# Kernel tuning notes

Measured on AMD Instinct MI355X. Metric: run time of the kernel, lower is better.

The kernel has to match this reference:

```python
import jax, jax.numpy as jnp
import numpy as np

N_CELLS = 10   # nr_cells
CELL = 20      # cell_size (w)
R = 1          # read heads
HID = 128      # controller hidden
IN = 10        # dnc input_size
OUT = 10       # output_dim
CLIP = 20.0
IFACE = R * CELL + 3 * CELL + 5 * R + 3  # 88


def _lstm_step(x, h, c, Wih, Whh, b):
    gates = x @ Wih.T + h @ Whh.T + b
    i, f, g, o = jnp.split(gates, 4, axis=-1)
    c = jax.nn.sigmoid(f) * c + jax.nn.sigmoid(i) * jnp.tanh(g)
    h = jax.nn.sigmoid(o) * jnp.tanh(c)
    return h, c


def _content(mem, keys, strengths):
    # mem (b,n,w), keys (b,k,w), strengths (b,k) -> (b,k,n)
    dot = jnp.einsum('bkw,bnw->bkn', keys, mem)
    kn = jnp.linalg.norm(keys, axis=-1, keepdims=True)
    mn = jnp.linalg.norm(mem, axis=-1)[:, None, :]
    return jax.nn.softmax(dot / (kn * mn + 1e-6) * strengths[..., None], axis=-1)


def _allocate(usage):
    u = 1e-6 + (1.0 - 1e-6) * usage
    idx = jnp.argsort(u, axis=-1)                      # ascending usage
    su = jnp.take_along_axis(u, idx, axis=-1)
    excl = jnp.concatenate([jnp.ones_like(su[:, :1]), jnp.cumprod(su, axis=-1)[:, :-1]], axis=-1)
    sa = (1.0 - su) * excl                             # sorted allocation weights
    inv = jnp.argsort(idx, axis=-1)
    return jnp.take_along_axis(sa, inv, axis=-1)


def _dnc_forward(x, W_ih0, W_hh0, b0, W_ih1, W_hh1, b1, W_if, b_if, W_out, b_out):
    B, T, _ = x.shape
    dt = x.dtype
    z = lambda *s: jnp.zeros(s, dt)
    carry0 = (z(B, HID), z(B, HID), z(B, HID), z(B, HID),   # h0,c0,h1,c1
              z(B, N_CELLS, CELL),                          # memory
              z(B, N_CELLS),                                # usage
              z(B, N_CELLS),                                # precedence
              z(B, N_CELLS, N_CELLS),                       # link matrix
              z(B, R, N_CELLS),                             # read weights
              z(B, N_CELLS),                                # write weights
              z(B, R, CELL))                                # read vectors
    eye = jnp.eye(N_CELLS, dtype=dt)

    def step(carry, xt):
        h0, c0, h1, c1, mem, usage, prec, link, rw, ww, rv = carry
        inp = jnp.concatenate([xt, rv.reshape(B, R * CELL)], axis=-1)
        h0, c0 = _lstm_step(inp, h0, c0, W_ih0, W_hh0, b0)
        h1, c1 = _lstm_step(h0, h1, c1, W_ih1, W_hh1, b1)
        ctrl = jnp.clip(h1, -CLIP, CLIP)
        xi = ctrl @ W_if.T + b_if                            # (B, 88)
        rk = jnp.tanh(xi[:, 0:20]).reshape(B, R, CELL)       # read keys
        rs = jax.nn.softplus(xi[:, 20:21])                   # read strengths
        wk = jnp.tanh(xi[:, 21:41]).reshape(B, 1, CELL)      # write key
        ws = jax.nn.softplus(xi[:, 41:42])                   # write strength
        er = jax.nn.sigmoid(xi[:, 42:62])                    # erase vector
        wv = jnp.tanh(xi[:, 62:82])                          # write vector
        fg = jax.nn.sigmoid(xi[:, 82:83])                    # free gates
        ga = jax.nn.sigmoid(xi[:, 83:84])                    # allocation gate
        gw = jax.nn.sigmoid(xi[:, 84:85])                    # write gate
        modes = jax.nn.softmax(xi[:, 85:88].reshape(B, R, 3), axis=-1)
        # --- write ---
        psi = jnp.prod(1.0 - fg[:, :, None] * rw, axis=1)    # retention (b,n)
        usage = (usage + ww - usage * ww) * psi
        alloc = _allocate(usage)
        cw = _content(mem, wk, ws)[:, 0]                     # (b,n)
        ww = gw * (ga * alloc + (1.0 - ga) * cw)
        mem = mem * (1.0 - ww[:, :, None] * er[:, None, :]) + ww[:, :, None] * wv[:, None, :]
        link = (1.0 - ww[:, :, None] - ww[:, None, :]) * link + ww[:, :, None] * prec[:, None, :]
        link = link * (1.0 - eye)
        prec = (1.0 - ww.sum(-1, keepdims=True)) * prec + ww
        # --- read ---
        fwd_w = jnp.einsum('brn,bmn->brm', rw, link)         # L @ w  (forward)
        bwd_w = jnp.einsum('brn,bnm->brm', rw, link)         # L^T @ w (backward)
        cr = _content(mem, rk, rs)
        rw = modes[..., 0:1] * bwd_w + modes[..., 1:2] * cr + modes[..., 2:3] * fwd_w
        rv = jnp.einsum('brn,bnw->brw', rw, mem)
        o = jnp.concatenate([ctrl, rv.reshape(B, R * CELL)], axis=-1)
        y = o @ W_out.T + b_out
        return (h0, c0, h1, c1, mem, usage, prec, link, rw, ww, rv), y

    _, ys = jax.lax.scan(step, carry0, jnp.swapaxes(x, 0, 1))
    return ys[-1]  # output[:, -1, :]


def setup_inputs() -> dict:
    key = jax.random.key(0)
    ks = jax.random.split(key, 8)
    s = 0.08
    B, T = 512, 512
    return {
        'x': jax.random.normal(ks[0], (B, T, IN), jnp.float32),
        'W_ih0': s * jax.random.normal(ks[1], (4 * HID, IN + R * CELL), jnp.float32),
        'W_hh0': s * jax.random.normal(ks[2], (4 * HID, HID), jnp.float32),
        'b0': jnp.zeros((4 * HID,), jnp.float32),
        'W_ih1': s * jax.random.normal(ks[3], (4 * HID, HID), jnp.float32),
        'W_hh1': s * jax.random.normal(ks[4], (4 * HID, HID), jnp.float32),
        'b1': jnp.zeros((4 * HID,), jnp.float32),
        'W_if': s * jax.random.normal(ks[5], (IFACE, HID), jnp.float32),
        'b_if': jnp.zeros((IFACE,), jnp.float32),
        'W_out': s * jax.random.normal(ks[6], (OUT, HID + R * CELL), jnp.float32),
        'b_out': jnp.zeros((OUT,), jnp.float32),
    }


def reference(x, W_ih0, W_hh0, b0, W_ih1, W_hh1, b1, W_if, b_if, W_out, b_out):
    return _dnc_forward(x, W_ih0, W_hh0, b0, W_ih1, W_hh1, b1, W_if, b_if, W_out, b_out)
```

## Files before the change

kernel.cpp:

```cpp
#include <hip/hip_runtime.h>
#include <math.h>

#define NT 512
#define NB 512
#define HID 128
#define NIN 10
#define NC 10
#define CW 20
#define NIF 88
#define NOUT 10
#define GB 16
#define BLK 512
#define NWG (NB/GB)

typedef _Float16 h1;
typedef _Float16 h8 __attribute__((ext_vector_type(8)));
typedef float f32x4 __attribute__((ext_vector_type(4)));

__device__ __forceinline__ float rcpf(float x) { return __builtin_amdgcn_rcpf(x); }
__device__ __forceinline__ float sigf(float x) { return rcpf(1.0f + __expf(-x)); }
__device__ __forceinline__ float tanhf_(float x) {
  float xc = fminf(fmaxf(x, -15.f), 15.f);
  float e = __expf(2.f * xc);
  return (e - 1.f) * rcpf(e + 1.f);
}
__device__ __forceinline__ float splus(float x) { return fmaxf(x, 0.0f) + __logf(1.f + __expf(-fabsf(x))); }

__device__ __forceinline__ float bq0(float v) { return __builtin_bit_cast(float, __builtin_amdgcn_ds_swizzle(__builtin_bit_cast(int, v), 0x001C)); }
__device__ __forceinline__ float bq1(float v) { return __builtin_bit_cast(float, __builtin_amdgcn_ds_swizzle(__builtin_bit_cast(int, v), 0x003C)); }
__device__ __forceinline__ float bq2(float v) { return __builtin_bit_cast(float, __builtin_amdgcn_ds_swizzle(__builtin_bit_cast(int, v), 0x005C)); }
__device__ __forceinline__ float bq3(float v) { return __builtin_bit_cast(float, __builtin_amdgcn_ds_swizzle(__builtin_bit_cast(int, v), 0x007C)); }

__device__ __forceinline__ f32x4 mfma16(float4 a, float4 b, f32x4 c) {
  return __builtin_amdgcn_mfma_f32_16x16x32_f16(
      __builtin_bit_cast(h8, a), __builtin_bit_cast(h8, b), c, 0, 0, 0);
}

__device__ __forceinline__ float4 pack8(const float* p) {
  h1 v[8];
  #pragma unroll
  for (int j = 0; j < 8; ++j) v[j] = (h1)p[j];
  return *reinterpret_cast<float4*>(v);
}

__device__ __host__ __forceinline__ int origrow(int prow) { return (prow & 3) * 128 + (prow >> 2); }

__global__ __launch_bounds__(256) void dnc_packf_kernel(
    const float* __restrict__ Whh0, const float* __restrict__ Wih1,
    const float* __restrict__ Whh1, float4* __restrict__ ws)
{
  int i = blockIdx.x * 256 + threadIdx.x;
  if (i >= 384 * 64) return;
  int l = i & 63, frag = i >> 6;
  int m = frag >> 7, f = frag & 127;
  int nt = f >> 2, kt = f & 3;
  int r = origrow(nt * 16 + (l & 15));
  int k0 = kt * 32 + (l >> 4) * 8;
  const float* W = (m == 0) ? Whh0 : (m == 1) ? Wih1 : Whh1;
  ws[i] = pack8(W + (size_t)r * HID + k0);
}

__global__ __launch_bounds__(BLK)
void dnc_mfma_kernel(
    const float* __restrict__ x,
    const float* __restrict__ Wih0, const float* __restrict__ Whh0, const float* __restrict__ b0,
    const float* __restrict__ Wih1, const float* __restrict__ Whh1, const float* __restrict__ b1,
    const float* __restrict__ Wif,  const float* __restrict__ bif,
    const float* __restrict__ Wout, const float* __restrict__ bout,
    const float4* __restrict__ wsT,
    float* __restrict__ out)
{
  __shared__ __align__(16) float4 s_w0f[32*64];
  __shared__ __align__(16) float4 s_wiff[24*64];
  __shared__ __align__(16) h1 s_h0f[16*16*8];
  __shared__ __align__(16) h1 s_h1f[16*16*8];
  __shared__ __align__(16) h1 s_ctf[16*16*8];
  __shared__ __align__(16) h1 s_inpf[4*16*8];
  __shared__ float s_c0[GB][HID], s_c1[GB][HID];
  __shared__ float s_ctrl32[GB][HID];
  __shared__ float s_mem[GB][NC][CW];
  __shared__ float s_link[GB][NC][NC];
  __shared__ float s_rk[GB][CW], s_wk[GB][CW], s_er[GB][CW], s_wv[GB][CW];
  __shared__ float s_sc[GB][8], s_mraw[GB][4];
  __shared__ float s_usage[GB][NC], s_u[GB][NC], s_prec[GB][NC], s_prec2[GB][NC];
  __shared__ float s_rw[GB][NC], s_ww[GB][NC], s_cw[GB][NC], s_cr[GB][NC];
  __shared__ float s_fwd[GB][NC], s_bwd[GB][NC];
  __shared__ float s_rv[GB][CW];

  const int tid = threadIdx.x;
  const int l = tid & 63, w = tid >> 6;
  const int col = l & 15, g4 = l >> 4, q4 = l & 3;
  const int bbase = blockIdx.x * GB;

  for (int idx = tid; idx < 32*64; idx += BLK) {
    int nt = idx >> 6, ll = idx & 63;
    int r = origrow(nt*16 + (ll & 15));
    int kg = ll >> 4;
    float tmp[8];
    #pragma unroll
    for (int j = 0; j < 8; ++j) {
      int k = kg*8 + j;
      int cc = (k < 10) ? k : ((k < 12) ? -1 : (k - 2));
      tmp[j] = (cc < 0) ? 0.f : Wih0[r*(NIN+CW) + cc];
    }
    s_w0f[idx] = pack8(tmp);
  }
  for (int idx = tid; idx < 24*64; idx += BLK) {
    int f = idx >> 6, ll = idx & 63;
    int nt = f >> 2, kt = f & 3;
    int q = nt*16 + (ll & 15);
    int k0 = kt*32 + (ll >> 4)*8;
    float tmp[8];
    #pragma unroll
    for (int j = 0; j < 8; ++j) tmp[j] = (q < NIF) ? Wif[q*HID + k0 + j] : 0.f;
    s_wiff[idx] = pack8(tmp);
  }
  for (int idx = tid; idx < 16*16*8; idx += BLK) {
    s_h0f[idx] = (h1)0.f; s_h1f[idx] = (h1)0.f; s_ctf[idx] = (h1)0.f;
  }
  if (tid < 4*16*8) s_inpf[tid] = (h1)0.f;
  for (int idx = tid; idx < GB*HID; idx += BLK) { int b = idx >> 7, u = idx & 127;
    s_c0[b][u] = 0.f; s_c1[b][u] = 0.f; s_ctrl32[b][u] = 0.f; }
  for (int idx = tid; idx < GB*NC*CW; idx += BLK) { int b = idx/(NC*CW), e = idx%(NC*CW);
    s_mem[b][e/CW][e%CW] = 0.f; }
  for (int idx = tid; idx < GB*NC*NC; idx += BLK) { int b = idx/(NC*NC), e = idx%(NC*NC);
    s_link[b][e/NC][e%NC] = 0.f; }
  if (tid < GB*NC) { int b = tid & 15, n = tid >> 4;
    s_usage[b][n] = 0.f; s_prec[b][n] = 0.f; s_rw[b][n] = 0.f; s_ww[b][n] = 0.f; }
  for (int idx = tid; idx < GB*CW; idx += BLK) { int b = idx/CW, c = idx%CW; s_rv[b][c] = 0.f; }
  if (tid < GB*NIN) { int b = tid/NIN, i = tid - b*NIN;
    float v = x[((size_t)(bbase+b)*NT + 0)*NIN + i];
    s_inpf[((i>>3)*16 + b)*8 + (i&7)] = (h1)v;
  }
  const float b0v0 = b0[origrow((w*4+0)*16+col)], b0v1 = b0[origrow((w*4+1)*16+col)];
  const float b0v2 = b0[origrow((w*4+2)*16+col)], b0v3 = b0[origrow((w*4+3)*16+col)];
  const float b1v0 = b1[origrow((w*4+0)*16+col)], b1v1 = b1[origrow((w*4+1)*16+col)];
  const float b1v2 = b1[origrow((w*4+2)*16+col)], b1v3 = b1[origrow((w*4+3)*16+col)];
  float bifv = 0.f;
  if (w < 6) { int q = w*16 + col; bifv = (q < NIF) ? bif[q] : 0.f; }
  __syncthreads();

  const float4* h0fp = (const float4*)s_h0f;
  const float4* h1fp = (const float4*)s_h1f;
  const float4* ctfp = (const float4*)s_ctf;
  const float4* inpfp = (const float4*)s_inpf;

  auto dnc_phases = [&](bool run) {
    if (run) {
      if (tid < GB*NC) {
        int b = tid & 15, n = tid >> 4;
        float fg = s_sc[b][2];
        float psi = 1.f - fg * s_rw[b][n];
        float u = s_usage[b][n], wq = s_ww[b][n];
        u = (u + wq - u*wq) * psi;
        s_usage[b][n] = u;
        s_u[b][n] = 1e-6f + (1.0f - 1e-6f) * u;
        float dot = 0.f, mn = 0.f, kn = 0.f;
        #pragma unroll
        for (int c = 0; c < CW; ++c) {
          float m = s_mem[b][n][c], k = s_wk[b][c];
          dot += k*m; mn += m*m; kn += k*k;
        }
        s_cw[b][n] = dot * rcpf(sqrtf(kn)*sqrtf(mn) + 1e-6f) * s_sc[b][1];
      } else if (tid < GB*NC + GB) {
        int b = tid - GB*NC;
        float m0 = s_mraw[b][0], m1 = s_mraw[b][1], m2 = s_mraw[b][2];
        float mm = fmaxf(m0, fmaxf(m1, m2));
        float e0 = __expf(m0-mm), e1 = __expf(m1-mm), e2 = __expf(m2-mm);
        float es = rcpf(e0+e1+e2);
        s_sc[b][5] = e0*es; s_sc[b][6] = e1*es; s_sc[b][7] = e2*es;
      }
    }
    __syncthreads();
    if (run && tid < GB*NC) {
      int b = tid & 15, n = tid >> 4;
      float mx = -1e30f;
      #pragma unroll
      for (int m = 0; m < NC; ++m) mx = fmaxf(mx, s_cw[b][m]);
      float sm = 0.f;
      #pragma unroll
      for (int m = 0; m < NC; ++m) sm += __expf(s_cw[b][m]-mx);
      float cwv = __expf(s_cw[b][n]-mx) * rcpf(sm);
      float un = s_u[b][n];
      float excl = 1.f;
      #pragma unroll
      for (int m = 0; m < NC; ++m) {
        float um = s_u[b][m];
        bool before = (um < un) || (um == un && m < n);
        excl *= before ? um : 1.f;
      }
      float alloc = (1.f - un) * excl;
      float ga = s_sc[b][3], gw = s_sc[b][4];
      s_ww[b][n] = gw * (ga*alloc + (1.f-ga)*cwv);
    }
    __syncthreads();
    if (run) {
      for (int e = tid; e < GB*NC*CW; e += BLK) {
        int b = e/(NC*CW), rr = (e/CW) % NC, c = e % CW;
        float wq = s_ww[b][rr];
        s_mem[b][rr][c] = s_mem[b][rr][c]*(1.f - wq*s_er[b][c]) + wq*s_wv[b][c];
      }
      for (int e = tid; e < GB*NC*NC; e += BLK) {
        int b = e/(NC*NC), i2 = (e/NC) % NC, j2 = e % NC;
        float wi = s_ww[b][i2], wj = s_ww[b][j2];
        float ln = (1.f - wi - wj)*s_link[b][i2][j2] + wi*s_prec[b][j2];
        s_link[b][i2][j2] = (i2==j2) ? 0.f : ln;
      }
      if (tid < GB*NC) {
        int b = tid & 15, n = tid >> 4;
        float sw2 = 0.f;
        #pragma unroll
        for (int m = 0; m < NC; ++m) sw2 += s_ww[b][m];
        s_prec2[b][n] = (1.f - sw2)*s_prec[b][n] + s_ww[b][n];
      }
    }
    __syncthreads();
    if (run) {
      if (tid < GB*NC) {
        int b = tid & 15, m = tid >> 4;
        s_prec[b][m] = s_prec2[b][m];
        float a = 0.f;
        #pragma unroll
        for (int n = 0; n < NC; ++n) a += s_rw[b][n]*s_link[b][m][n];
        s_fwd[b][m] = a;
      } else if (tid < 2*GB*NC) {
        int tt = tid - GB*NC, b = tt & 15, m = tt >> 4;
        float a = 0.f;
        #pragma unroll
        for (int n = 0; n < NC; ++n) a += s_rw[b][n]*s_link[b][n][m];
        s_bwd[b][m] = a;
      } else if (tid < 3*GB*NC) {
        int tt = tid - 2*GB*NC, b = tt & 15, n = tt >> 4;
        float dot = 0.f, mn = 0.f, kn = 0.f;
        #pragma unroll
        for (int c = 0; c < CW; ++c) {
          float m = s_mem[b][n][c], k = s_rk[b][c];
          dot += k*m; mn += m*m; kn += k*k;
        }
        s_cr[b][n] = dot * rcpf(sqrtf(kn)*sqrtf(mn) + 1e-6f) * s_sc[b][0];
      }
    }
    __syncthreads();
    if (run && tid < GB*NC) {
      int b = tid & 15, n = tid >> 4;
      float mx = -1e30f;
      #pragma unroll
      for (int m = 0; m < NC; ++m) mx = fmaxf(mx, s_cr[b][m]);
      float sm = 0.f;
      #pragma unroll
      for (int m = 0; m < NC; ++m) sm += __expf(s_cr[b][m]-mx);
      float cr = __expf(s_cr[b][n]-mx)*rcpf(sm);
      s_rw[b][n] = s_sc[b][5]*s_bwd[b][n] + s_sc[b][6]*cr + s_sc[b][7]*s_fwd[b][n];
    }
    __syncthreads();
    if (run && tid < GB*CW) {
      int b = tid & 15, c = tid >> 4;
      float a = 0.f;
      #pragma unroll
      for (int n = 0; n < NC; ++n) a += s_rw[b][n]*s_mem[b][n][c];
      s_rv[b][c] = a;
      int k = 12 + c;
      s_inpf[((k>>3)*16 + b)*8 + (k&7)] = (h1)a;
    }
    __syncthreads();
  };

  auto lstm_layer = [&](f32x4 ac0, f32x4 ac1, f32x4 ac2, f32x4 ac3,
                        float (*cst)[HID], h1* hf, bool isL1) {
    float GI[4] = {0,0,0,0}, GF[4] = {0,0,0,0}, GG[4] = {0,0,0,0}, GO[4] = {0,0,0,0};
    #pragma unroll
    for (int r = 0; r < 4; ++r) {
      f32x4 A = (r==0) ? ac0 : (r==1) ? ac1 : (r==2) ? ac2 : ac3;
      #pragma unroll
      for (int i = 0; i < 4; ++i) {
        float t0 = bq0(A[i]), t1 = bq1(A[i]), t2 = bq2(A[i]), t3 = bq3(A[i]);
        GI[i] = (q4 == r) ? t0 : GI[i];
        GF[i] = (q4 == r) ? t1 : GF[i];
        GG[i] = (q4 == r) ? t2 : GG[i];
        GO[i] = (q4 == r) ? t3 : GO[i];
      }
    }
    const int u = (w*4 + q4)*4 + (col >> 2);
    #pragma unroll
    for (int i = 0; i < 4; ++i) {
      int b = g4*4 + i;
      float c = sigf(GF[i])*cst[b][u] + sigf(GI[i])*tanhf_(GG[i]);
      cst[b][u] = c;
      float h = sigf(GO[i])*tanhf_(c);
      hf[((u>>3)*16 + b)*8 + (u&7)] = (h1)h;
      if (isL1) {
        float cl = fminf(fmaxf(h, -20.f), 20.f);
        s_ctf[((u>>3)*16 + b)*8 + (u&7)] = (h1)cl;
        s_ctrl32[b][u] = cl;
      }
    }
  };

  for (int t = 0; t < NT; ++t) {
    dnc_phases(t > 0);

    unsigned lnd = 0;
    asm volatile("" : "+v"(lnd));
    const float4* WS = (const float4*)((const char*)wsT + lnd);

    float4 ai  = inpfp[g4*16 + col];
    float4 a00 = h0fp[(0*4+g4)*16 + col], a01 = h0fp[(1*4+g4)*16 + col];
    float4 a02 = h0fp[(2*4+g4)*16 + col], a03 = h0fp[(3*4+g4)*16 + col];
    float4 a10 = h1fp[(0*4+g4)*16 + col], a11 = h1fp[(1*4+g4)*16 + col];
    float4 a12 = h1fp[(2*4+g4)*16 + col], a13 = h1fp[(3*4+g4)*16 + col];

    f32x4 acc0 = {b0v0,b0v0,b0v0,b0v0}, acc1 = {b0v1,b0v1,b0v1,b0v1};
    f32x4 acc2 = {b0v2,b0v2,b0v2,b0v2}, acc3 = {b0v3,b0v3,b0v3,b0v3};
    f32x4 gcc0 = {b1v0,b1v0,b1v0,b1v0}, gcc1 = {b1v1,b1v1,b1v1,b1v1};
    f32x4 gcc2 = {b1v2,b1v2,b1v2,b1v2}, gcc3 = {b1v3,b1v3,b1v3,b1v3};

#define G0IT(ACC, IT)                                                   \
    ACC = mfma16(ai,  s_w0f[(w*4+IT)*64 + l], ACC);                     \
    ACC = mfma16(a00, WS[((w*4+IT)*4+0)*64 + l], ACC);                  \
    ACC = mfma16(a01, WS[((w*4+IT)*4+1)*64 + l], ACC);                  \
    ACC = mfma16(a02, WS[((w*4+IT)*4+2)*64 + l], ACC);                  \
    ACC = mfma16(a03, WS[((w*4+IT)*4+3)*64 + l], ACC);
    G0IT(acc0, 0) G0IT(acc1, 1) G0IT(acc2, 2) G0IT(acc3, 3)
#undef G0IT
#define G1H1(ACC, IT)                                                   \
    ACC = mfma16(a10, WS[(256+(w*4+IT)*4+0)*64 + l], ACC);              \
    ACC = mfma16(a11, WS[(256+(w*4+IT)*4+1)*64 + l], ACC);              \
    ACC = mfma16(a12, WS[(256+(w*4+IT)*4+2)*64 + l], ACC);              \
    ACC = mfma16(a13, WS[(256+(w*4+IT)*4+3)*64 + l], ACC);
    G1H1(gcc0, 0) G1H1(gcc1, 1) G1H1(gcc2, 2) G1H1(gcc3, 3)
#undef G1H1
    __syncthreads();

    lstm_layer(acc0, acc1, acc2, acc3, s_c0, s_h0f, false);
    __syncthreads();

    {
      float4 ah0 = h0fp[(0*4+g4)*16 + col], ah1 = h0fp[(1*4+g4)*16 + col];
      float4 ah2 = h0fp[(2*4+g4)*16 + col], ah3 = h0fp[(3*4+g4)*16 + col];
#define G1H0(ACC, IT)                                                   \
      ACC = mfma16(ah0, WS[(128+(w*4+IT)*4+0)*64 + l], ACC);            \
      ACC = mfma16(ah1, WS[(128+(w*4+IT)*4+1)*64 + l], ACC);            \
      ACC = mfma16(ah2, WS[(128+(w*4+IT)*4+2)*64 + l], ACC);            \
      ACC = mfma16(ah3, WS[(128+(w*4+IT)*4+3)*64 + l], ACC);
      G1H0(gcc0, 0) G1H0(gcc1, 1) G1H0(gcc2, 2) G1H0(gcc3, 3)
#undef G1H0
      lstm_layer(gcc0, gcc1, gcc2, gcc3, s_c1, s_h1f, true);
    }
    __syncthreads();

    if (w < 6) {
      float4 ac0 = ctfp[(0*4+g4)*16 + col], ac1 = ctfp[(1*4+g4)*16 + col];
      float4 ac2 = ctfp[(2*4+g4)*16 + col], ac3 = ctfp[(3*4+g4)*16 + col];
      f32x4 acc = {bifv, bifv, bifv, bifv};
      acc = mfma16(ac0, s_wiff[(w*4+0)*64 + l], acc);
      acc = mfma16(ac1, s_wiff[(w*4+1)*64 + l], acc);
      acc = mfma16(ac2, s_wiff[(w*4+2)*64 + l], acc);
      acc = mfma16(ac3, s_wiff[(w*4+3)*64 + l], acc);
      int q = w*16 + col;
      if (q < NIF) {
        #pragma unroll
        for (int i = 0; i < 4; ++i) {
          float a = acc[i];
          int b = g4*4 + i;
          if      (q < 20)  s_rk[b][q]    = tanhf_(a);
          else if (q == 20) s_sc[b][0]    = splus(a);
          else if (q < 41)  s_wk[b][q-21] = tanhf_(a);
          else if (q == 41) s_sc[b][1]    = splus(a);
          else if (q < 62)  s_er[b][q-42] = sigf(a);
          else if (q < 82)  s_wv[b][q-62] = tanhf_(a);
          else if (q == 82) s_sc[b][2]    = sigf(a);
          else if (q == 83) s_sc[b][3]    = sigf(a);
          else if (q == 84) s_sc[b][4]    = sigf(a);
          else              s_mraw[b][q-85] = a;
        }
      }
    } else {
      for (int e = (w-6)*64 + l; e < GB*NIN; e += 128) {
        int b = e/NIN, i = e - b*NIN;
        if (t+1 < NT) {
          float v = x[((size_t)(bbase+b)*NT + (t+1))*NIN + i];
          s_inpf[((i>>3)*16 + b)*8 + (i&7)] = (h1)v;
        }
      }
    }
    __syncthreads();
  }

  dnc_phases(true);

  if (tid < GB*NOUT) {
    int b = tid & 15, o = tid >> 4;
    float a = bout[o];
    const float* Wr = Wout + o*(HID+CW);
    #pragma unroll 4
    for (int k = 0; k < HID; ++k) a += Wr[k]*s_ctrl32[b][k];
    #pragma unroll
    for (int c = 0; c < CW; ++c) a += Wr[HID+c]*s_rv[b][c];
    out[(size_t)(bbase+b)*NOUT + o] = a;
  }
}

extern "C" void kernel_launch(void* const* d_in, const int* in_sizes, int n_in,
                              void* d_out, int out_size, void* d_ws, size_t ws_size,
                              hipStream_t stream) {
  (void)in_sizes; (void)n_in; (void)out_size; (void)ws_size;
  const float* x    = (const float*)d_in[0];
  const float* Wih0 = (const float*)d_in[1];
  const float* Whh0 = (const float*)d_in[2];
  const float* b0   = (const float*)d_in[3];
  const float* Wih1 = (const float*)d_in[4];
  const float* Whh1 = (const float*)d_in[5];
  const float* b1   = (const float*)d_in[6];
  const float* Wif  = (const float*)d_in[7];
  const float* bif  = (const float*)d_in[8];
  const float* Wout = (const float*)d_in[9];
  const float* bout = (const float*)d_in[10];
  float* out = (float*)d_out;
  float4* ws = (float4*)d_ws;

  dnc_packf_kernel<<<dim3(96), dim3(256), 0, stream>>>(Whh0, Wih1, Whh1, ws);
  dnc_mfma_kernel<<<dim3(NWG), dim3(BLK), 0, stream>>>(
      x, Wih0, Whh0, b0, Wih1, Whh1, b1, Wif, bif, Wout, bout, ws, out);
}
```

Measured before the change: 5.543 ms.

## Interleave per-wave DNC memory phases with LSTM MFMA recurrences, replacing block barriers

```diff
diff --git a/kernel.cpp b/kernel.cpp
--- a/kernel.cpp
+++ b/kernel.cpp
@@ -30,6 +30,9 @@
 __device__ __forceinline__ float bq1(float v) { return __builtin_bit_cast(float, __builtin_amdgcn_ds_swizzle(__builtin_bit_cast(int, v), 0x003C)); }
 __device__ __forceinline__ float bq2(float v) { return __builtin_bit_cast(float, __builtin_amdgcn_ds_swizzle(__builtin_bit_cast(int, v), 0x005C)); }
 __device__ __forceinline__ float bq3(float v) { return __builtin_bit_cast(float, __builtin_amdgcn_ds_swizzle(__builtin_bit_cast(int, v), 0x007C)); }
+
+#define LDSFENCE() do { asm volatile("s_waitcnt lgkmcnt(0)" ::: "memory"); \
+                        __builtin_amdgcn_sched_barrier(0); } while (0)
 
 __device__ __forceinline__ f32x4 mfma16(float4 a, float4 b, f32x4 c) {
   return __builtin_amdgcn_mfma_f32_16x16x32_f16(
@@ -61,7 +64,7 @@
 }
 
 __global__ __launch_bounds__(BLK)
-void dnc_mfma_kernel(
+void dnc_olap2_kernel(
     const float* __restrict__ x,
     const float* __restrict__ Wih0, const float* __restrict__ Whh0, const float* __restrict__ b0,
     const float* __restrict__ Wih1, const float* __restrict__ Whh1, const float* __restrict__ b1,
@@ -91,6 +94,7 @@
   const int l = tid & 63, w = tid >> 6;
   const int col = l & 15, g4 = l >> 4, q4 = l & 3;
   const int bbase = blockIdx.x * GB;
+  const int s = l & 31, bb = 2 * w + (l >> 5);
 
   for (int idx = tid; idx < 32*64; idx += BLK) {
     int nt = idx >> 6, ll = idx & 63;
@@ -145,124 +149,121 @@
   const float4* ctfp = (const float4*)s_ctf;
   const float4* inpfp = (const float4*)s_inpf;
 
-  auto dnc_phases = [&](bool run) {
-    if (run) {
-      if (tid < GB*NC) {
-        int b = tid & 15, n = tid >> 4;
-        float fg = s_sc[b][2];
-        float psi = 1.f - fg * s_rw[b][n];
-        float u = s_usage[b][n], wq = s_ww[b][n];
-        u = (u + wq - u*wq) * psi;
-        s_usage[b][n] = u;
-        s_u[b][n] = 1e-6f + (1.0f - 1e-6f) * u;
-        float dot = 0.f, mn = 0.f, kn = 0.f;
-        #pragma unroll
-        for (int c = 0; c < CW; ++c) {
-          float m = s_mem[b][n][c], k = s_wk[b][c];
-          dot += k*m; mn += m*m; kn += k*k;
-        }
-        s_cw[b][n] = dot * rcpf(sqrtf(kn)*sqrtf(mn) + 1e-6f) * s_sc[b][1];
-      } else if (tid < GB*NC + GB) {
-        int b = tid - GB*NC;
-        float m0 = s_mraw[b][0], m1 = s_mraw[b][1], m2 = s_mraw[b][2];
-        float mm = fmaxf(m0, fmaxf(m1, m2));
-        float e0 = __expf(m0-mm), e1 = __expf(m1-mm), e2 = __expf(m2-mm);
-        float es = rcpf(e0+e1+e2);
-        s_sc[b][5] = e0*es; s_sc[b][6] = e1*es; s_sc[b][7] = e2*es;
-      }
-    }
-    __syncthreads();
-    if (run && tid < GB*NC) {
-      int b = tid & 15, n = tid >> 4;
+  auto dncH = [&]() {
+    if (s < NC) {
+      int n = s;
+      float fg = s_sc[bb][2];
+      float psi = 1.f - fg * s_rw[bb][n];
+      float u = s_usage[bb][n], wq = s_ww[bb][n];
+      u = (u + wq - u*wq) * psi;
+      s_usage[bb][n] = u;
+      s_u[bb][n] = 1e-6f + (1.0f - 1e-6f) * u;
+      float dot = 0.f, mn = 0.f, kn = 0.f;
+      #pragma unroll
+      for (int c = 0; c < CW; ++c) {
+        float mv = s_mem[bb][n][c], kv = s_wk[bb][c];
+        dot += kv*mv; mn += mv*mv; kn += kv*kv;
+      }
+      s_cw[bb][n] = dot * rcpf(sqrtf(kn)*sqrtf(mn) + 1e-6f) * s_sc[bb][1];
+    } else if (s == NC) {
+      float m0 = s_mraw[bb][0], m1 = s_mraw[bb][1], m2 = s_mraw[bb][2];
+      float mm = fmaxf(m0, fmaxf(m1, m2));
+      float e0 = __expf(m0-mm), e1 = __expf(m1-mm), e2 = __expf(m2-mm);
+      float es = rcpf(e0+e1+e2);
+      s_sc[bb][5] = e0*es; s_sc[bb][6] = e1*es; s_sc[bb][7] = e2*es;
+    }
+  };
+  auto dncI = [&]() {
+    if (s < NC) {
+      int n = s;
       float mx = -1e30f;
       #pragma unroll
-      for (int m = 0; m < NC; ++m) mx = fmaxf(mx, s_cw[b][m]);
+      for (int m = 0; m < NC; ++m) mx = fmaxf(mx, s_cw[bb][m]);
       float sm = 0.f;
       #pragma unroll
-      for (int m = 0; m < NC; ++m) sm += __expf(s_cw[b][m]-mx);
-      float cwv = __expf(s_cw[b][n]-mx) * rcpf(sm);
-      float un = s_u[b][n];
+      for (int m = 0; m < NC; ++m) sm += __expf(s_cw[bb][m]-mx);
+      float cwv = __expf(s_cw[bb][n]-mx) * rcpf(sm);
+      float un = s_u[bb][n];
       float excl = 1.f;
       #pragma unroll
       for (int m = 0; m < NC; ++m) {
-        float um = s_u[b][m];
+        float um = s_u[bb][m];
         bool before = (um < un) || (um == un && m < n);
         excl *= before ? um : 1.f;
       }
       float alloc = (1.f - un) * excl;
-      float ga = s_sc[b][3], gw = s_sc[b][4];
-      s_ww[b][n] = gw * (ga*alloc + (1.f-ga)*cwv);
-    }
-    __syncthreads();
-    if (run) {
-      for (int e = tid; e < GB*NC*CW; e += BLK) {
-        int b = e/(NC*CW), rr = (e/CW) % NC, c = e % CW;
-        float wq = s_ww[b][rr];
-        s_mem[b][rr][c] = s_mem[b][rr][c]*(1.f - wq*s_er[b][c]) + wq*s_wv[b][c];
-      }
-      for (int e = tid; e < GB*NC*NC; e += BLK) {
-        int b = e/(NC*NC), i2 = (e/NC) % NC, j2 = e % NC;
-        float wi = s_ww[b][i2], wj = s_ww[b][j2];
-        float ln = (1.f - wi - wj)*s_link[b][i2][j2] + wi*s_prec[b][j2];
-        s_link[b][i2][j2] = (i2==j2) ? 0.f : ln;
-      }
-      if (tid < GB*NC) {
-        int b = tid & 15, n = tid >> 4;
-        float sw2 = 0.f;
-        #pragma unroll
-        for (int m = 0; m < NC; ++m) sw2 += s_ww[b][m];
-        s_prec2[b][n] = (1.f - sw2)*s_prec[b][n] + s_ww[b][n];
-      }
-    }
-    __syncthreads();
-    if (run) {
-      if (tid < GB*NC) {
-        int b = tid & 15, m = tid >> 4;
-        s_prec[b][m] = s_prec2[b][m];
-        float a = 0.f;
-        #pragma unroll
-        for (int n = 0; n < NC; ++n) a += s_rw[b][n]*s_link[b][m][n];
-        s_fwd[b][m] = a;
-      } else if (tid < 2*GB*NC) {
-        int tt = tid - GB*NC, b = tt & 15, m = tt >> 4;
-        float a = 0.f;
-        #pragma unroll
-        for (int n = 0; n < NC; ++n) a += s_rw[b][n]*s_link[b][n][m];
-        s_bwd[b][m] = a;
-      } else if (tid < 3*GB*NC) {
-        int tt = tid - 2*GB*NC, b = tt & 15, n = tt >> 4;
-        float dot = 0.f, mn = 0.f, kn = 0.f;
-        #pragma unroll
-        for (int c = 0; c < CW; ++c) {
-          float m = s_mem[b][n][c], k = s_rk[b][c];
-          dot += k*m; mn += m*m; kn += k*k;
-        }
-        s_cr[b][n] = dot * rcpf(sqrtf(kn)*sqrtf(mn) + 1e-6f) * s_sc[b][0];
-      }
-    }
-    __syncthreads();
-    if (run && tid < GB*NC) {
-      int b = tid & 15, n = tid >> 4;
+      float ga = s_sc[bb][3], gw = s_sc[bb][4];
+      s_ww[bb][n] = gw * (ga*alloc + (1.f-ga)*cwv);
+    }
+  };
+  auto dncJ = [&]() {
+    #pragma unroll
+    for (int e = s; e < NC*CW; e += 32) {
+      int rr = e/CW, c = e%CW;
+      float wq = s_ww[bb][rr];
+      s_mem[bb][rr][c] = s_mem[bb][rr][c]*(1.f - wq*s_er[bb][c]) + wq*s_wv[bb][c];
+    }
+    #pragma unroll
+    for (int e = s; e < NC*NC; e += 32) {
+      int i2 = e/NC, j2 = e%NC;
+      float wi = s_ww[bb][i2], wj = s_ww[bb][j2];
+      float ln = (1.f - wi - wj)*s_link[bb][i2][j2] + wi*s_prec[bb][j2];
+      s_link[bb][i2][j2] = (i2==j2) ? 0.f : ln;
+    }
+    if (s < NC) {
+      float sw2 = 0.f;
+      #pragma unroll
+      for (int m = 0; m < NC; ++m) sw2 += s_ww[bb][m];
+      s_prec2[bb][s] = (1.f - sw2)*s_prec[bb][s] + s_ww[bb][s];
+    }
+  };
+  auto dncK = [&]() {
+    if (s < NC) {
+      int m = s;
+      s_prec[bb][m] = s_prec2[bb][m];
+      float a = 0.f;
+      #pragma unroll
+      for (int n = 0; n < NC; ++n) a += s_rw[bb][n]*s_link[bb][m][n];
+      s_fwd[bb][m] = a;
+    } else if (s < 2*NC) {
+      int m = s - NC;
+      float a = 0.f;
+      #pragma unroll
+      for (int n = 0; n < NC; ++n) a += s_rw[bb][n]*s_link[bb][n][m];
+      s_bwd[bb][m] = a;
+    } else if (s < 3*NC) {
+      int n = s - 2*NC;
+      float dot = 0.f, mn = 0.f, kn = 0.f;
+      #pragma unroll
+      for (int c = 0; c < CW; ++c) {
+        float mv = s_mem[bb][n][c], kv = s_rk[bb][c];
+        dot += kv*mv; mn += mv*mv; kn += kv*kv;
+      }
+      s_cr[bb][n] = dot * rcpf(sqrtf(kn)*sqrtf(mn) + 1e-6f) * s_sc[bb][0];
+    }
+  };
+  auto dncL = [&]() {
+    if (s < NC) {
+      int n = s;
       float mx = -1e30f;
       #pragma unroll
-      for (int m = 0; m < NC; ++m) mx = fmaxf(mx, s_cr[b][m]);
+      for (int m = 0; m < NC; ++m) mx = fmaxf(mx, s_cr[bb][m]);
       float sm = 0.f;
       #pragma unroll
-      for (int m = 0; m < NC; ++m) sm += __expf(s_cr[b][m]-mx);
-      float cr = __expf(s_cr[b][n]-mx)*rcpf(sm);
-      s_rw[b][n] = s_sc[b][5]*s_bwd[b][n] + s_sc[b][6]*cr + s_sc[b][7]*s_fwd[b][n];
-    }
-    __syncthreads();
-    if (run && tid < GB*CW) {
-      int b = tid & 15, c = tid >> 4;
+      for (int m = 0; m < NC; ++m) sm += __expf(s_cr[bb][m]-mx);
+      float cr = __expf(s_cr[bb][n]-mx)*rcpf(sm);
+      s_rw[bb][n] = s_sc[bb][5]*s_bwd[bb][n] + s_sc[bb][6]*cr + s_sc[bb][7]*s_fwd[bb][n];
+    }
+  };
+  auto dncM = [&]() {
+    if (s < CW) {
       float a = 0.f;
       #pragma unroll
-      for (int n = 0; n < NC; ++n) a += s_rw[b][n]*s_mem[b][n][c];
-      s_rv[b][c] = a;
-      int k = 12 + c;
-      s_inpf[((k>>3)*16 + b)*8 + (k&7)] = (h1)a;
-    }
-    __syncthreads();
+      for (int n = 0; n < NC; ++n) a += s_rw[bb][n]*s_mem[bb][n][s];
+      s_rv[bb][s] = a;
+      int k = 12 + s;
+      s_inpf[((k>>3)*16 + bb)*8 + (k&7)] = (h1)a;
+    }
   };
 
   auto lstm_layer = [&](f32x4 ac0, f32x4 ac1, f32x4 ac2, f32x4 ac3,
@@ -296,56 +297,78 @@
     }
   };
 
+#define LDG(B0,B1,B2,B3, FB) { B0 = WS[((FB)+0)*64+l]; B1 = WS[((FB)+1)*64+l]; \
+                               B2 = WS[((FB)+2)*64+l]; B3 = WS[((FB)+3)*64+l]; }
+#define MMAH0(ACC,B0,B1,B2,B3) { \
+  { float4 a_ = h0fp[(0*4+g4)*16+col]; ACC = mfma16(a_, B0, ACC); } \
+  { float4 a_ = h0fp[(1*4+g4)*16+col]; ACC = mfma16(a_, B1, ACC); } \
+  { float4 a_ = h0fp[(2*4+g4)*16+col]; ACC = mfma16(a_, B2, ACC); } \
+  { float4 a_ = h0fp[(3*4+g4)*16+col]; ACC = mfma16(a_, B3, ACC); } }
+#define MMAH1(ACC,B0,B1,B2,B3) { \
+  { float4 a_ = h1fp[(0*4+g4)*16+col]; ACC = mfma16(a_, B0, ACC); } \
+  { float4 a_ = h1fp[(1*4+g4)*16+col]; ACC = mfma16(a_, B1, ACC); } \
+  { float4 a_ = h1fp[(2*4+g4)*16+col]; ACC = mfma16(a_, B2, ACC); } \
+  { float4 a_ = h1fp[(3*4+g4)*16+col]; ACC = mfma16(a_, B3, ACC); } }
+
   for (int t = 0; t < NT; ++t) {
-    dnc_phases(t > 0);
-
     unsigned lnd = 0;
     asm volatile("" : "+v"(lnd));
     const float4* WS = (const float4*)((const char*)wsT + lnd);
 
-    float4 ai  = inpfp[g4*16 + col];
-    float4 a00 = h0fp[(0*4+g4)*16 + col], a01 = h0fp[(1*4+g4)*16 + col];
-    float4 a02 = h0fp[(2*4+g4)*16 + col], a03 = h0fp[(3*4+g4)*16 + col];
-    float4 a10 = h1fp[(0*4+g4)*16 + col], a11 = h1fp[(1*4+g4)*16 + col];
-    float4 a12 = h1fp[(2*4+g4)*16 + col], a13 = h1fp[(3*4+g4)*16 + col];
-
-    f32x4 acc0 = {b0v0,b0v0,b0v0,b0v0}, acc1 = {b0v1,b0v1,b0v1,b0v1};
-    f32x4 acc2 = {b0v2,b0v2,b0v2,b0v2}, acc3 = {b0v3,b0v3,b0v3,b0v3};
-    f32x4 gcc0 = {b1v0,b1v0,b1v0,b1v0}, gcc1 = {b1v1,b1v1,b1v1,b1v1};
-    f32x4 gcc2 = {b1v2,b1v2,b1v2,b1v2}, gcc3 = {b1v3,b1v3,b1v3,b1v3};
-
-#define G0IT(ACC, IT)                                                   \
-    ACC = mfma16(ai,  s_w0f[(w*4+IT)*64 + l], ACC);                     \
-    ACC = mfma16(a00, WS[((w*4+IT)*4+0)*64 + l], ACC);                  \
-    ACC = mfma16(a01, WS[((w*4+IT)*4+1)*64 + l], ACC);                  \
-    ACC = mfma16(a02, WS[((w*4+IT)*4+2)*64 + l], ACC);                  \
-    ACC = mfma16(a03, WS[((w*4+IT)*4+3)*64 + l], ACC);
-    G0IT(acc0, 0) G0IT(acc1, 1) G0IT(acc2, 2) G0IT(acc3, 3)
-#undef G0IT
-#define G1H1(ACC, IT)                                                   \
-    ACC = mfma16(a10, WS[(256+(w*4+IT)*4+0)*64 + l], ACC);              \
-    ACC = mfma16(a11, WS[(256+(w*4+IT)*4+1)*64 + l], ACC);              \
-    ACC = mfma16(a12, WS[(256+(w*4+IT)*4+2)*64 + l], ACC);              \
-    ACC = mfma16(a13, WS[(256+(w*4+IT)*4+3)*64 + l], ACC);
-    G1H1(gcc0, 0) G1H1(gcc1, 1) G1H1(gcc2, 2) G1H1(gcc3, 3)
-#undef G1H1
+    f32x4 g00 = {b0v0,b0v0,b0v0,b0v0}, g01 = {b0v1,b0v1,b0v1,b0v1};
+    f32x4 g02 = {b0v2,b0v2,b0v2,b0v2}, g03 = {b0v3,b0v3,b0v3,b0v3};
+    f32x4 g10 = {b1v0,b1v0,b1v0,b1v0}, g11 = {b1v1,b1v1,b1v1,b1v1};
+    f32x4 g12 = {b1v2,b1v2,b1v2,b1v2}, g13 = {b1v3,b1v3,b1v3,b1v3};
+    float4 P0,P1,P2,P3, Q0,Q1,Q2,Q3;
+    LDG(P0,P1,P2,P3, (w*4+0)*4)
+    LDG(Q0,Q1,Q2,Q3, (w*4+1)*4)
+    if (t > 0) dncH();
+    LDSFENCE();
+    MMAH0(g00, P0,P1,P2,P3)
+    LDG(P0,P1,P2,P3, (w*4+2)*4)
+    if (t > 0) dncI();
+    LDSFENCE();
+    MMAH0(g01, Q0,Q1,Q2,Q3)
+    LDG(Q0,Q1,Q2,Q3, (w*4+3)*4)
+    if (t > 0) dncJ();
+    LDSFENCE();
+    MMAH0(g02, P0,P1,P2,P3)
+    LDG(P0,P1,P2,P3, 256 + (w*4+0)*4)
+    if (t > 0) dncK();
+    LDSFENCE();
+    MMAH0(g03, Q0,Q1,Q2,Q3)
+    LDG(Q0,Q1,Q2,Q3, 256 + (w*4+1)*4)
+    if (t > 0) dncL();
+    LDSFENCE();
+    MMAH1(g10, P0,P1,P2,P3)
+    LDG(P0,P1,P2,P3, 256 + (w*4+2)*4)
+    if (t > 0) dncM();
+    LDSFENCE();
+    MMAH1(g11, Q0,Q1,Q2,Q3)
+    LDG(Q0,Q1,Q2,Q3, 256 + (w*4+3)*4)
+    MMAH1(g12, P0,P1,P2,P3)
+    MMAH1(g13, Q0,Q1,Q2,Q3)
     __syncthreads();
 
-    lstm_layer(acc0, acc1, acc2, acc3, s_c0, s_h0f, false);
+    {
+      float4 ainp = inpfp[g4*16 + col];
+      g00 = mfma16(ainp, s_w0f[(w*4+0)*64 + l], g00);
+      g01 = mfma16(ainp, s_w0f[(w*4+1)*64 + l], g01);
+      g02 = mfma16(ainp, s_w0f[(w*4+2)*64 + l], g02);
+      g03 = mfma16(ainp, s_w0f[(w*4+3)*64 + l], g03);
+      lstm_layer(g00, g01, g02, g03, s_c0, s_h0f, false);
+    }
     __syncthreads();
 
-    {
-      float4 ah0 = h0fp[(0*4+g4)*16 + col], ah1 = h0fp[(1*4+g4)*16 + col];
-      float4 ah2 = h0fp[(2*4+g4)*16 + col], ah3 = h0fp[(3*4+g4)*16 + col];
-#define G1H0(ACC, IT)                                                   \
-      ACC = mfma16(ah0, WS[(128+(w*4+IT)*4+0)*64 + l], ACC);            \
-      ACC = mfma16(ah1, WS[(128+(w*4+IT)*4+1)*64 + l], ACC);            \
-      ACC = mfma16(ah2, WS[(128+(w*4+IT)*4+2)*64 + l], ACC);            \
-      ACC = mfma16(ah3, WS[(128+(w*4+IT)*4+3)*64 + l], ACC);
-      G1H0(gcc0, 0) G1H0(gcc1, 1) G1H0(gcc2, 2) G1H0(gcc3, 3)
-#undef G1H0
-      lstm_layer(gcc0, gcc1, gcc2, gcc3, s_c1, s_h1f, true);
-    }
+    LDG(P0,P1,P2,P3, 128 + (w*4+0)*4)
+    LDG(Q0,Q1,Q2,Q3, 128 + (w*4+1)*4)
+    MMAH0(g10, P0,P1,P2,P3)
+    LDG(P0,P1,P2,P3, 128 + (w*4+2)*4)
+    MMAH0(g11, Q0,Q1,Q2,Q3)
+    LDG(Q0,Q1,Q2,Q3, 128 + (w*4+3)*4)
+    MMAH0(g12, P0,P1,P2,P3)
+    MMAH0(g13, Q0,Q1,Q2,Q3)
+    lstm_layer(g10, g11, g12, g13, s_c1, s_h1f, true);
     __syncthreads();
 
     if (w < 6) {
@@ -386,7 +409,13 @@
     __syncthreads();
   }
 
-  dnc_phases(true);
+  dncH(); LDSFENCE();
+  dncI(); LDSFENCE();
+  dncJ(); LDSFENCE();
+  dncK(); LDSFENCE();
+  dncL(); LDSFENCE();
+  dncM();
+  __syncthreads();
 
   if (tid < GB*NOUT) {
     int b = tid & 15, o = tid >> 4;
@@ -398,6 +427,9 @@
     for (int c = 0; c < CW; ++c) a += Wr[HID+c]*s_rv[b][c];
     out[(size_t)(bbase+b)*NOUT + o] = a;
   }
+#undef LDG
+#undef MMAH0
+#undef MMAH1
 }
 
 extern "C" void kernel_launch(void* const* d_in, const int* in_sizes, int n_in,
@@ -419,6 +451,6 @@
   float4* ws = (float4*)d_ws;
 
   dnc_packf_kernel<<<dim3(96), dim3(256), 0, stream>>>(Whh0, Wih1, Whh1, ws);
-  dnc_mfma_kernel<<<dim3(NWG), dim3(BLK), 0, stream>>>(
+  dnc_olap2_kernel<<<dim3(NWG), dim3(BLK), 0, stream>>>(
       x, Wih0, Whh0, b0, Wih1, Whh1, b1, Wif, bif, Wout, bout, ws, out);
 }
```

New measurement: 5.314 ms. 1.04x faster.
